# Optimization experiments

Measured on AMD Instinct MI355X. Metric: run time of the kernel, lower is better.

The kernel has to match this reference:

```python
import jax, jax.numpy as jnp
import numpy as np

B, T, N, D = 4, 12, 512, 128
L = 4            # max_lag + 1 lag encoders
H = D // 2       # lag-encoder hidden dim
THRESHOLD = 0.1


def setup_inputs() -> dict:
    key = jax.random.key(0)
    ks = jax.random.split(key, 10)
    s = 0.02
    return {
        "x":   jax.random.normal(ks[0], (B, T, N, D), dtype=jnp.float32),
        # lag encoders: Linear(D->H), ReLU, Linear(H->D), stacked over L lags
        "W1":  s * jax.random.normal(ks[1], (L, D, H), dtype=jnp.float32),
        "b1":  jnp.zeros((L, H), dtype=jnp.float32),
        "W2":  s * jax.random.normal(ks[2], (L, H, D), dtype=jnp.float32),
        "b2":  jnp.zeros((L, D), dtype=jnp.float32),
        # causal scorer: Linear(2D->D), ReLU, (Dropout=id in eval), Linear(D->1), Sigmoid
        "Ws1": s * jax.random.normal(ks[3], (2 * D, D), dtype=jnp.float32),
        "bs1": jnp.zeros((D,), dtype=jnp.float32),
        "Ws2": s * jax.random.normal(ks[4], (D, 1), dtype=jnp.float32),
        "bs2": jnp.zeros((1,), dtype=jnp.float32),
    }


def reference(x, W1, b1, W2, b2, Ws1, bs1, Ws2, bs2):
    Tdim = x.shape[1]
    # lagged slices x[:, T-1-lag] for lag in 0..L-1 (all lags active since T > max_lag)
    lags = jnp.stack([x[:, max(0, Tdim - 1 - l)] for l in range(L)], axis=1)  # (B,L,N,D)
    h = jax.nn.relu(jnp.einsum('blnd,ldh->blnh', lags, W1) + b1[None, :, None, :])
    enc = jnp.einsum('blnh,lhd->blnd', h, W2) + b2[None, :, None, :]          # (B,L,N,D)
    agg = enc.mean(axis=1)                                                    # (B,N,D)

    # pairwise causal scorer. cat([src, tgt]) @ Ws1 == src @ Ws1[:D] + tgt @ Ws1[D:],
    # avoiding the explicit (B,N,N,2D) concat.
    src_proj = jnp.einsum('bnd,dk->bnk', agg, Ws1[:D])   # (B,N,D)
    tgt_proj = jnp.einsum('bnd,dk->bnk', agg, Ws1[D:])   # (B,N,D)
    pre = src_proj[:, :, None, :] + tgt_proj[:, None, :, :] + bs1  # (B,N,N,D)
    score = jax.nn.sigmoid(jnp.einsum('bijd,d->bij', jax.nn.relu(pre), Ws2[:, 0]) + bs2[0])

    # threshold sparsification + remove self loops
    adj = jnp.where(score > THRESHOLD, score, 0.0)
    adj = adj * (1.0 - jnp.eye(N, dtype=adj.dtype))

    # multi-hop propagation and global max normalization per batch element
    a2 = jnp.matmul(adj, adj)
    a3 = jnp.matmul(a2, adj)
    enhanced = adj + 0.5 * a2 + 0.25 * a3
    mx = jnp.max(enhanced, axis=(-1, -2), keepdims=True)
    return enhanced / (mx + 1e-8)
```

## Files before the change

### kernel.cpp

```cpp
#include <hip/hip_runtime.h>
#include <math.h>

#define Bn 4
#define Tn 12
#define Nn 512
#define Dn 128
#define Ln 4
#define Hn 64
#define NNe (Nn*Nn)

typedef __attribute__((ext_vector_type(8))) short short8;
typedef __attribute__((ext_vector_type(4))) float f32x4;

__device__ __forceinline__ unsigned short f2bf(float f) {
    unsigned int u = __float_as_uint(f);
    unsigned int r = (u + 0x7FFF + ((u >> 16) & 1)) >> 16;
    return (unsigned short)r;
}
__device__ __forceinline__ float bf2f(unsigned short s) {
    return __uint_as_float(((unsigned int)s) << 16);
}

__global__ __launch_bounds__(256) void k_enc_a(
    const float* __restrict__ x, const float* __restrict__ W1, const float* __restrict__ b1,
    unsigned short* __restrict__ hb, unsigned int* __restrict__ maxslot)
{
    __shared__ __align__(16) unsigned short xA[32*136];
    __shared__ __align__(16) unsigned short w1T[64*136];
    int tid = threadIdx.x;
    int rg = blockIdx.x, lag = blockIdx.y;
    if (rg == 0 && lag == 0 && tid < Bn) maxslot[tid] = 0u;
    int r0 = rg * 32;
    int bb = r0 >> 9, n0 = r0 & 511;

    {
        const float4* xs = (const float4*)(x + ((size_t)(bb*Tn + (Tn-1-lag))*Nn + n0)*Dn);
        for (int v = tid; v < 1024; v += 256) {
            float4 f = xs[v];
            int row = v >> 5, c4 = v & 31;
            ushort4 o = { f2bf(f.x), f2bf(f.y), f2bf(f.z), f2bf(f.w) };
            *(ushort4*)&xA[row*136 + c4*4] = o;
        }
    }
    {
        int n = tid & 63, kq = tid >> 6;
        const float* Wp = W1 + (size_t)lag*Dn*Hn;
        #pragma unroll
        for (int r = 0; r < 4; ++r) {
            int k0 = (r*4 + kq)*8;
            unsigned short tmp[8];
            #pragma unroll
            for (int j = 0; j < 8; ++j) tmp[j] = f2bf(Wp[(size_t)(k0+j)*Hn + n]);
            *(short8*)&w1T[n*136 + k0] = *(const short8*)tmp;
        }
    }
    __syncthreads();

    int wv = __builtin_amdgcn_readfirstlane(tid >> 6);
    int lane = tid & 63;
    int wm = wv >> 1, wn = wv & 1;
    int m = lane & 15, q = lane >> 4;
    f32x4 acc[2] = {{0.f,0.f,0.f,0.f},{0.f,0.f,0.f,0.f}};
    #pragma unroll
    for (int ks = 0; ks < 4; ++ks) {
        short8 af = *(const short8*)&xA[(wm*16 + m)*136 + ks*32 + q*8];
        #pragma unroll
        for (int nt = 0; nt < 2; ++nt) {
            short8 bg = *(const short8*)&w1T[(wn*32 + nt*16 + m)*136 + ks*32 + q*8];
            acc[nt] = __builtin_amdgcn_mfma_f32_16x16x32_bf16(af, bg, acc[nt], 0, 0, 0);
        }
    }
    int colL = lane & 15, rq = lane >> 4;
    #pragma unroll
    for (int nt = 0; nt < 2; ++nt) {
        int ncol = wn*32 + nt*16 + colL;
        float bv = b1[lag*Hn + ncol];
        #pragma unroll
        for (int reg = 0; reg < 4; ++reg) {
            int rowL = wm*16 + rq*4 + reg;
            hb[(size_t)(r0+rowL)*256 + lag*64 + ncol] = f2bf(fmaxf(acc[nt][reg] + bv, 0.f));
        }
    }
}

__global__ __launch_bounds__(256) void k_enc_bc(
    const unsigned short* __restrict__ hb, const float* __restrict__ W2,
    const float* __restrict__ b2, const float* __restrict__ Ws1,
    const float* __restrict__ bs1,
    unsigned short* __restrict__ spb, unsigned short* __restrict__ tpb)
{
    __shared__ __align__(16) unsigned short hA[16*264];
    __shared__ __align__(16) unsigned short wT[64*264];
    __shared__ __align__(16) unsigned short aggA[16*136];
    int tid = threadIdx.x;
    int wv = __builtin_amdgcn_readfirstlane(tid >> 6);
    int lane = tid & 63;
    int r0 = blockIdx.x * 16;

    for (int v = tid; v < 512; v += 256) {
        int row = v >> 5, c = v & 31;
        *(short8*)&hA[row*264 + c*8] = *(const short8*)(hb + (size_t)(r0+row)*256 + c*8);
    }

    int m = lane & 15, q = lane >> 4;
    int colL = lane & 15, rq = lane >> 4;

    for (int ch = 0; ch < 2; ++ch) {
        __syncthreads();
        {
            int n = tid & 63, kq = tid >> 6;
            #pragma unroll
            for (int r = 0; r < 8; ++r) {
                int k0 = (r*4 + kq)*8;
                unsigned short tmp[8];
                #pragma unroll
                for (int j = 0; j < 8; ++j) tmp[j] = f2bf(W2[(size_t)(k0+j)*Dn + ch*64 + n]);
                *(short8*)&wT[n*264 + k0] = *(const short8*)tmp;
            }
        }
        __syncthreads();
        f32x4 acc = {0.f,0.f,0.f,0.f};
        #pragma unroll
        for (int ks = 0; ks < 8; ++ks) {
            short8 af = *(const short8*)&hA[m*264 + ks*32 + q*8];
            short8 bg = *(const short8*)&wT[(wv*16 + m)*264 + ks*32 + q*8];
            acc = __builtin_amdgcn_mfma_f32_16x16x32_bf16(af, bg, acc, 0, 0, 0);
        }
        int col = ch*64 + wv*16 + colL;
        float b2s = b2[col] + b2[Dn+col] + b2[2*Dn+col] + b2[3*Dn+col];
        #pragma unroll
        for (int reg = 0; reg < 4; ++reg)
            aggA[(rq*4+reg)*136 + col] = f2bf(0.25f*(acc[reg] + b2s));
    }

    for (int tgt = 0; tgt < 2; ++tgt) {
        __syncthreads();
        {
            int n = tid & 127, kq = tid >> 7;
            #pragma unroll
            for (int r = 0; r < 8; ++r) {
                int k0 = (r*2 + kq)*8;
                unsigned short tmp[8];
                #pragma unroll
                for (int j = 0; j < 8; ++j)
                    tmp[j] = f2bf(Ws1[(size_t)(tgt*Dn + k0 + j)*Dn + n]);
                *(short8*)&wT[n*136 + k0] = *(const short8*)tmp;
            }
        }
        __syncthreads();
        f32x4 acc[2] = {{0.f,0.f,0.f,0.f},{0.f,0.f,0.f,0.f}};
        #pragma unroll
        for (int ks = 0; ks < 4; ++ks) {
            short8 af = *(const short8*)&aggA[m*136 + ks*32 + q*8];
            #pragma unroll
            for (int nt = 0; nt < 2; ++nt) {
                short8 bg = *(const short8*)&wT[(wv*32 + nt*16 + m)*136 + ks*32 + q*8];
                acc[nt] = __builtin_amdgcn_mfma_f32_16x16x32_bf16(af, bg, acc[nt], 0, 0, 0);
            }
        }
        unsigned short* dst = tgt ? tpb : spb;
        #pragma unroll
        for (int nt = 0; nt < 2; ++nt) {
            int n = wv*32 + nt*16 + colL;
            float bv = tgt ? 0.f : bs1[n];
            #pragma unroll
            for (int reg = 0; reg < 4; ++reg)
                dst[(size_t)(r0 + rq*4 + reg)*Dn + n] = f2bf(acc[nt][reg] + bv);
        }
    }
}

__global__ __launch_bounds__(256) void k_score(
    const unsigned short* __restrict__ spb, const unsigned short* __restrict__ tpb,
    const float* __restrict__ Ws2, const float* __restrict__ bs2,
    unsigned short* __restrict__ adj_b, unsigned short* __restrict__ adj_bt)
{
    __shared__ float spl[64*132];
    __shared__ unsigned short tplT[Dn*72];
    int tid = threadIdx.x;
    int wv = __builtin_amdgcn_readfirstlane(tid >> 6);
    int lane = tid & 63;
    int bz = blockIdx.z;
    int i0b = blockIdx.y * 64, j0b = blockIdx.x * 64;
    const unsigned short* spr = spb + (size_t)bz*Nn*Dn;
    const unsigned short* tpr = tpb + (size_t)bz*Nn*Dn;

    for (int v = tid; v < 1024; v += 256) {
        int row = v >> 4, c = v & 15;
        const unsigned short* src = spr + (size_t)(i0b+row)*Dn + c*8;
        ushort4 u0 = *(const ushort4*)src;
        ushort4 u1 = *(const ushort4*)(src + 4);
        float4 f0 = { bf2f(u0.x), bf2f(u0.y), bf2f(u0.z), bf2f(u0.w) };
        float4 f1 = { bf2f(u1.x), bf2f(u1.y), bf2f(u1.z), bf2f(u1.w) };
        *(float4*)&spl[row*132 + c*8]     = f0;
        *(float4*)&spl[row*132 + c*8 + 4] = f1;
    }
    {
        int j = tid & 63, kq = tid >> 6;
        for (int p = 0; p < 4; ++p) {
            int k8 = p*4 + kq;
            short8 tv = *(const short8*)(tpr + (size_t)(j0b+j)*Dn + k8*8);
            #pragma unroll
            for (int t = 0; t < 8; ++t) tplT[(k8*8+t)*72 + j] = (unsigned short)tv[t];
        }
    }
    __syncthreads();

    int iq = lane >> 4, jq = lane & 15;
    int iw = wv*16 + iq*4;
    float acc[4][4] = {};
    for (int k8 = 0; k8 < 16; ++k8) {
        float4 wa = *(const float4*)(Ws2 + k8*8);
        float4 wb = *(const float4*)(Ws2 + k8*8 + 4);
        float4 sA[4], sB[4];
        #pragma unroll
        for (int ii = 0; ii < 4; ++ii) {
            sA[ii] = *(const float4*)&spl[(iw+ii)*132 + k8*8];
            sB[ii] = *(const float4*)&spl[(iw+ii)*132 + k8*8 + 4];
        }
        ushort4 t4[8];
        #pragma unroll
        for (int kk = 0; kk < 8; ++kk) t4[kk] = *(const ushort4*)&tplT[(k8*8+kk)*72 + jq*4];
        #pragma unroll
        for (int kk = 0; kk < 8; ++kk) {
            float w = (kk < 4) ? ((const float*)&wa)[kk] : ((const float*)&wb)[kk-4];
            float tv0 = bf2f(t4[kk].x), tv1 = bf2f(t4[kk].y);
            float tv2 = bf2f(t4[kk].z), tv3 = bf2f(t4[kk].w);
            #pragma unroll
            for (int ii = 0; ii < 4; ++ii) {
                float s = (kk < 4) ? ((const float*)&sA[ii])[kk] : ((const float*)&sB[ii])[kk-4];
                acc[ii][0] += fmaxf(s + tv0, 0.f)*w;
                acc[ii][1] += fmaxf(s + tv1, 0.f)*w;
                acc[ii][2] += fmaxf(s + tv2, 0.f)*w;
                acc[ii][3] += fmaxf(s + tv3, 0.f)*w;
            }
        }
    }
    float bsv = bs2[0];
    int i0 = i0b + iw;
    int j0 = j0b + jq*4;
    float vals[4][4];
    #pragma unroll
    for (int ii = 0; ii < 4; ++ii) {
        int i = i0 + ii;
        #pragma unroll
        for (int jj = 0; jj < 4; ++jj) {
            float z = acc[ii][jj] + bsv;
            float sc = 1.f/(1.f + __expf(-z));
            int j = j0 + jj;
            vals[ii][jj] = (sc > 0.1f && i != j) ? sc : 0.f;
        }
    }
    size_t base = (size_t)bz << 18;
    #pragma unroll
    for (int ii = 0; ii < 4; ++ii) {
        ushort4 rv = make_ushort4(f2bf(vals[ii][0]), f2bf(vals[ii][1]),
                                  f2bf(vals[ii][2]), f2bf(vals[ii][3]));
        *(ushort4*)(adj_b + base + (size_t)(i0+ii)*Nn + j0) = rv;
    }
    #pragma unroll
    for (int jj = 0; jj < 4; ++jj) {
        ushort4 cv = make_ushort4(f2bf(vals[0][jj]), f2bf(vals[1][jj]),
                                  f2bf(vals[2][jj]), f2bf(vals[3][jj]));
        *(ushort4*)(adj_bt + base + (size_t)(j0+jj)*Nn + i0) = cv;
    }
}

__global__ __launch_bounds__(256) void k_mm1(
    const unsigned short* __restrict__ adj_b, const unsigned short* __restrict__ adj_bt,
    unsigned short* __restrict__ a2b)
{
    __shared__ unsigned short Als[64*72];
    __shared__ unsigned short Bls[64*72];
    int tid = threadIdx.x;
    int wv = __builtin_amdgcn_readfirstlane(tid >> 6);
    int lane = tid & 63;
    int b = blockIdx.z, i0 = blockIdx.y*64, j0 = blockIdx.x*64;
    size_t base = (size_t)b << 18;
    const unsigned short* Ab = adj_b + base;
    const unsigned short* Bb = adj_bt + base;
    int wm = wv >> 1, wn = wv & 1;
    int m = lane & 15, q = lane >> 4;
    int sr = tid >> 2, sc = (tid & 3)*16;
    f32x4 acc[2][2];
    #pragma unroll
    for (int mt = 0; mt < 2; ++mt)
        #pragma unroll
        for (int nt = 0; nt < 2; ++nt) acc[mt][nt] = (f32x4){0.f,0.f,0.f,0.f};
    short8 pa0, pa1, pb0, pb1;
    pa0 = *(const short8*)(Ab + (size_t)(i0+sr)*Nn + sc);
    pa1 = *(const short8*)(Ab + (size_t)(i0+sr)*Nn + sc + 8);
    pb0 = *(const short8*)(Bb + (size_t)(j0+sr)*Nn + sc);
    pb1 = *(const short8*)(Bb + (size_t)(j0+sr)*Nn + sc + 8);
    for (int kt = 0; kt < 8; ++kt) {
        *(short8*)&Als[sr*72 + sc]     = pa0;
        *(short8*)&Als[sr*72 + sc + 8] = pa1;
        *(short8*)&Bls[sr*72 + sc]     = pb0;
        *(short8*)&Bls[sr*72 + sc + 8] = pb1;
        __syncthreads();
        if (kt < 7) {
            int k0 = (kt+1)*64;
            pa0 = *(const short8*)(Ab + (size_t)(i0+sr)*Nn + k0 + sc);
            pa1 = *(const short8*)(Ab + (size_t)(i0+sr)*Nn + k0 + sc + 8);
            pb0 = *(const short8*)(Bb + (size_t)(j0+sr)*Nn + k0 + sc);
            pb1 = *(const short8*)(Bb + (size_t)(j0+sr)*Nn + k0 + sc + 8);
        }
        #pragma unroll
        for (int ks = 0; ks < 2; ++ks) {
            short8 af[2], bg[2];
            #pragma unroll
            for (int mt = 0; mt < 2; ++mt) af[mt] = *(const short8*)&Als[(wm*32+mt*16+m)*72 + ks*32 + q*8];
            #pragma unroll
            for (int nt = 0; nt < 2; ++nt) bg[nt] = *(const short8*)&Bls[(wn*32+nt*16+m)*72 + ks*32 + q*8];
            #pragma unroll
            for (int mt = 0; mt < 2; ++mt)
                #pragma unroll
                for (int nt = 0; nt < 2; ++nt)
                    acc[mt][nt] = __builtin_amdgcn_mfma_f32_16x16x32_bf16(af[mt], bg[nt], acc[mt][nt], 0, 0, 0);
        }
        __syncthreads();
    }
    int col = lane & 15, rq = lane >> 4;
    #pragma unroll
    for (int mt = 0; mt < 2; ++mt)
        #pragma unroll
        for (int nt = 0; nt < 2; ++nt)
            #pragma unroll
            for (int reg = 0; reg < 4; ++reg) {
                int i = i0 + wm*32 + mt*16 + rq*4 + reg;
                int j = j0 + wn*32 + nt*16 + col;
                a2b[base + (size_t)i*Nn + j] = f2bf(acc[mt][nt][reg]);
            }
}

__global__ __launch_bounds__(256) void k_mm2(
    const unsigned short* __restrict__ adj_b, const unsigned short* __restrict__ adj_bt,
    const unsigned short* __restrict__ a2b,
    float* __restrict__ out, unsigned int* __restrict__ maxslot)
{
    __shared__ unsigned short Als[64*72];
    __shared__ unsigned short Bls[64*72];
    __shared__ float red[4];
    int tid = threadIdx.x;
    int wv = __builtin_amdgcn_readfirstlane(tid >> 6);
    int lane = tid & 63;
    int b = blockIdx.z, i0 = blockIdx.y*64, j0 = blockIdx.x*64;
    size_t base = (size_t)b << 18;
    const unsigned short* Ab = a2b + base;
    const unsigned short* Bb = adj_bt + base;
    int wm = wv >> 1, wn = wv & 1;
    int m = lane & 15, q = lane >> 4;
    int sr = tid >> 2, sc = (tid & 3)*16;
    f32x4 acc[2][2];
    #pragma unroll
    for (int mt = 0; mt < 2; ++mt)
        #pragma unroll
        for (int nt = 0; nt < 2; ++nt) acc[mt][nt] = (f32x4){0.f,0.f,0.f,0.f};
    short8 pa0, pa1, pb0, pb1;
    pa0 = *(const short8*)(Ab + (size_t)(i0+sr)*Nn + sc);
    pa1 = *(const short8*)(Ab + (size_t)(i0+sr)*Nn + sc + 8);
    pb0 = *(const short8*)(Bb + (size_t)(j0+sr)*Nn + sc);
    pb1 = *(const short8*)(Bb + (size_t)(j0+sr)*Nn + sc + 8);
    for (int kt = 0; kt < 8; ++kt) {
        *(short8*)&Als[sr*72 + sc]     = pa0;
        *(short8*)&Als[sr*72 + sc + 8] = pa1;
        *(short8*)&Bls[sr*72 + sc]     = pb0;
        *(short8*)&Bls[sr*72 + sc + 8] = pb1;
        __syncthreads();
        if (kt < 7) {
            int k0 = (kt+1)*64;
            pa0 = *(const short8*)(Ab + (size_t)(i0+sr)*Nn + k0 + sc);
            pa1 = *(const short8*)(Ab + (size_t)(i0+sr)*Nn + k0 + sc + 8);
            pb0 = *(const short8*)(Bb + (size_t)(j0+sr)*Nn + k0 + sc);
            pb1 = *(const short8*)(Bb + (size_t)(j0+sr)*Nn + k0 + sc + 8);
        }
        #pragma unroll
        for (int ks = 0; ks < 2; ++ks) {
            short8 af[2], bg[2];
            #pragma unroll
            for (int mt = 0; mt < 2; ++mt) af[mt] = *(const short8*)&Als[(wm*32+mt*16+m)*72 + ks*32 + q*8];
            #pragma unroll
            for (int nt = 0; nt < 2; ++nt) bg[nt] = *(const short8*)&Bls[(wn*32+nt*16+m)*72 + ks*32 + q*8];
            #pragma unroll
            for (int mt = 0; mt < 2; ++mt)
                #pragma unroll
                for (int nt = 0; nt < 2; ++nt)
                    acc[mt][nt] = __builtin_amdgcn_mfma_f32_16x16x32_bf16(af[mt], bg[nt], acc[mt][nt], 0, 0, 0);
        }
        __syncthreads();
    }
    int col = lane & 15, rq = lane >> 4;
    float lmax = 0.f;
    const unsigned short* adjp = adj_b + base;
    #pragma unroll
    for (int mt = 0; mt < 2; ++mt)
        #pragma unroll
        for (int nt = 0; nt < 2; ++nt)
            #pragma unroll
            for (int reg = 0; reg < 4; ++reg) {
                int i = i0 + wm*32 + mt*16 + rq*4 + reg;
                int j = j0 + wn*32 + nt*16 + col;
                size_t off = (size_t)i*Nn + j;
                float e = bf2f(adjp[off]) + 0.5f*bf2f(Ab[off]) + 0.25f*acc[mt][nt][reg];
                out[base + off] = e;
                lmax = fmaxf(lmax, e);
            }
    #pragma unroll
    for (int s = 1; s < 64; s <<= 1) lmax = fmaxf(lmax, __shfl_xor(lmax, s, 64));
    if (lane == 0) red[wv] = lmax;
    __syncthreads();
    if (tid == 0) {
        float mx = fmaxf(fmaxf(red[0], red[1]), fmaxf(red[2], red[3]));
        atomicMax(maxslot + b, __float_as_uint(mx));
    }
}

__global__ __launch_bounds__(256) void k_norm(float* __restrict__ out,
                                              const unsigned int* __restrict__ maxslot)
{
    int idx = blockIdx.x*256 + threadIdx.x;
    int b = idx >> 16;
    float m = __uint_as_float(maxslot[b]);
    float inv = 1.f/(m + 1e-8f);
    float4* p = (float4*)out + idx;
    float4 v = *p;
    v.x *= inv; v.y *= inv; v.z *= inv; v.w *= inv;
    *p = v;
}

extern "C" void kernel_launch(void* const* d_in, const int* in_sizes, int n_in,
                              void* d_out, int out_size, void* d_ws, size_t ws_size,
                              hipStream_t stream) {
    const float* x   = (const float*)d_in[0];
    const float* W1  = (const float*)d_in[1];
    const float* b1  = (const float*)d_in[2];
    const float* W2  = (const float*)d_in[3];
    const float* b2  = (const float*)d_in[4];
    const float* Ws1 = (const float*)d_in[5];
    const float* bs1 = (const float*)d_in[6];
    const float* Ws2 = (const float*)d_in[7];
    const float* bs2 = (const float*)d_in[8];
    float* out = (float*)d_out;

    unsigned char* wsb = (unsigned char*)d_ws;
    unsigned short* spb    = (unsigned short*)(wsb);
    unsigned short* tpb    = (unsigned short*)(wsb + (512u<<10));
    unsigned short* adj_b  = (unsigned short*)(wsb + (1024u<<10));
    unsigned short* adj_bt = (unsigned short*)(wsb + (3072u<<10));
    unsigned short* a2b    = (unsigned short*)(wsb + (5120u<<10));
    unsigned int*   maxslot= (unsigned int*)(wsb + (7168u<<10));
    unsigned short* hb     = (unsigned short*)(wsb + (7172u<<10));

    k_enc_a <<<dim3(64, 4),   256, 0, stream>>>(x, W1, b1, hb, maxslot);
    k_enc_bc<<<dim3(128),     256, 0, stream>>>(hb, W2, b2, Ws1, bs1, spb, tpb);
    k_score <<<dim3(8, 8, Bn),256, 0, stream>>>(spb, tpb, Ws2, bs2, adj_b, adj_bt);
    k_mm1   <<<dim3(8, 8, Bn),256, 0, stream>>>(adj_b, adj_bt, a2b);
    k_mm2   <<<dim3(8, 8, Bn),256, 0, stream>>>(adj_b, adj_bt, a2b, out, maxslot);
    k_norm  <<<dim3(1024),    256, 0, stream>>>(out, maxslot);
}
```

Baseline: 124.4 us.

## Fuse all stages into one cooperative persistent kernel with grid syncs

Replaces six separate kernel launches with a single cooperative kernel of 256 blocks that runs the encoder, scorer, two adjacency matmuls and normalization as phases separated by grid-wide syncs. The encoder's first layer is also fused with the second, so the hidden activations stay in LDS instead of making a round trip through global memory. The aim is to remove launch gaps and inter-kernel tail effects. In exchange, only 128 blocks do work in the encoder phase, and each grid sync adds barrier cost.

```diff
diff --git a/kernel.cpp b/kernel.cpp
--- a/kernel.cpp
+++ b/kernel.cpp
@@ -1,5 +1,8 @@
 #include <hip/hip_runtime.h>
+#include <hip/hip_cooperative_groups.h>
 #include <math.h>
+
+namespace cg = cooperative_groups;
 
 #define Bn 4
 #define Tn 12
@@ -7,7 +10,6 @@
 #define Dn 128
 #define Ln 4
 #define Hn 64
-#define NNe (Nn*Nn)
 
 typedef __attribute__((ext_vector_type(8))) short short8;
 typedef __attribute__((ext_vector_type(4))) float f32x4;
@@ -21,411 +23,380 @@
     return __uint_as_float(((unsigned int)s) << 16);
 }
 
-__global__ __launch_bounds__(256) void k_enc_a(
-    const float* __restrict__ x, const float* __restrict__ W1, const float* __restrict__ b1,
-    unsigned short* __restrict__ hb, unsigned int* __restrict__ maxslot)
+__global__ __launch_bounds__(256) void k_all(
+    const float* __restrict__ x,  const float* __restrict__ W1, const float* __restrict__ b1,
+    const float* __restrict__ W2, const float* __restrict__ b2,
+    const float* __restrict__ Ws1, const float* __restrict__ bs1,
+    const float* __restrict__ Ws2, const float* __restrict__ bs2,
+    unsigned short* __restrict__ spb, unsigned short* __restrict__ tpb,
+    unsigned short* __restrict__ adj_b, unsigned short* __restrict__ adj_bt,
+    unsigned short* __restrict__ a2b,
+    unsigned int* __restrict__ maxslot, float* __restrict__ out)
 {
-    __shared__ __align__(16) unsigned short xA[32*136];
-    __shared__ __align__(16) unsigned short w1T[64*136];
-    int tid = threadIdx.x;
-    int rg = blockIdx.x, lag = blockIdx.y;
-    if (rg == 0 && lag == 0 && tid < Bn) maxslot[tid] = 0u;
-    int r0 = rg * 32;
-    int bb = r0 >> 9, n0 = r0 & 511;
+    __shared__ __align__(16) unsigned char ldsraw[52224];
+    cg::grid_group gg = cg::this_grid();
+    int tid  = threadIdx.x;
+    int bid  = blockIdx.x;
+    int wv   = __builtin_amdgcn_readfirstlane(tid >> 6);
+    int lane = tid & 63;
+
+    if (bid == 0 && tid < Bn)
+        __hip_atomic_store(maxslot + tid, 0u, __ATOMIC_RELAXED, __HIP_MEMORY_SCOPE_AGENT);
+
+    if (bid < 128) {
+        unsigned short* hA   = (unsigned short*)ldsraw;
+        unsigned short* wT   = (unsigned short*)(ldsraw + 8448);
+        unsigned short* aggA = (unsigned short*)(ldsraw + 43264);
+        unsigned short* xA   = aggA;
+        int r0 = bid * 16;
+        int bb = r0 >> 9, n0 = r0 & 511;
+        int m = lane & 15, q = lane >> 4;
+        int colL = lane & 15, rq = lane >> 4;
+
+        for (int lag = 0; lag < Ln; ++lag) {
+            __syncthreads();
+            {
+                const float4* xs = (const float4*)(x + ((size_t)(bb*Tn + (Tn-1-lag))*Nn + n0)*Dn);
+                for (int v = tid; v < 512; v += 256) {
+                    float4 f = xs[v];
+                    int row = v >> 5, c4 = v & 31;
+                    ushort4 o = { f2bf(f.x), f2bf(f.y), f2bf(f.z), f2bf(f.w) };
+                    *(ushort4*)&xA[row*136 + c4*4] = o;
+                }
+            }
+            {
+                int n = tid & 63, kq = tid >> 6;
+                const float* Wp = W1 + (size_t)lag*Dn*Hn;
+                #pragma unroll
+                for (int r = 0; r < 4; ++r) {
+                    int k0 = (r*4 + kq)*8;
+                    unsigned short tmp[8];
+                    #pragma unroll
+                    for (int j = 0; j < 8; ++j) tmp[j] = f2bf(Wp[(size_t)(k0+j)*Hn + n]);
+                    *(short8*)&wT[n*136 + k0] = *(const short8*)tmp;
+                }
+            }
+            __syncthreads();
+            f32x4 acc = {0.f,0.f,0.f,0.f};
+            #pragma unroll
+            for (int ks = 0; ks < 4; ++ks) {
+                short8 af = *(const short8*)&xA[m*136 + ks*32 + q*8];
+                short8 bg = *(const short8*)&wT[(wv*16 + m)*136 + ks*32 + q*8];
+                acc = __builtin_amdgcn_mfma_f32_16x16x32_bf16(af, bg, acc, 0, 0, 0);
+            }
+            int ncol = wv*16 + colL;
+            float bv = b1[lag*Hn + ncol];
+            #pragma unroll
+            for (int reg = 0; reg < 4; ++reg)
+                hA[(rq*4+reg)*264 + lag*64 + ncol] = f2bf(fmaxf(acc[reg] + bv, 0.f));
+        }
+
+        for (int ch = 0; ch < 2; ++ch) {
+            __syncthreads();
+            {
+                int n = tid & 63, kq = tid >> 6;
+                #pragma unroll
+                for (int r = 0; r < 8; ++r) {
+                    int k0 = (r*4 + kq)*8;
+                    unsigned short tmp[8];
+                    #pragma unroll
+                    for (int j = 0; j < 8; ++j) tmp[j] = f2bf(W2[(size_t)(k0+j)*Dn + ch*64 + n]);
+                    *(short8*)&wT[n*264 + k0] = *(const short8*)tmp;
+                }
+            }
+            __syncthreads();
+            f32x4 acc = {0.f,0.f,0.f,0.f};
+            #pragma unroll
+            for (int ks = 0; ks < 8; ++ks) {
+                short8 af = *(const short8*)&hA[m*264 + ks*32 + q*8];
+                short8 bg = *(const short8*)&wT[(wv*16 + m)*264 + ks*32 + q*8];
+                acc = __builtin_amdgcn_mfma_f32_16x16x32_bf16(af, bg, acc, 0, 0, 0);
+            }
+            int col = ch*64 + wv*16 + colL;
+            float b2s = b2[col] + b2[Dn+col] + b2[2*Dn+col] + b2[3*Dn+col];
+            #pragma unroll
+            for (int reg = 0; reg < 4; ++reg)
+                aggA[(rq*4+reg)*136 + col] = f2bf(0.25f*(acc[reg] + b2s));
+        }
+
+        for (int tgt = 0; tgt < 2; ++tgt) {
+            __syncthreads();
+            {
+                int n = tid & 127, kq = tid >> 7;
+                #pragma unroll
+                for (int r = 0; r < 8; ++r) {
+                    int k0 = (r*2 + kq)*8;
+                    unsigned short tmp[8];
+                    #pragma unroll
+                    for (int j = 0; j < 8; ++j)
+                        tmp[j] = f2bf(Ws1[(size_t)(tgt*Dn + k0 + j)*Dn + n]);
+                    *(short8*)&wT[n*136 + k0] = *(const short8*)tmp;
+                }
+            }
+            __syncthreads();
+            f32x4 acc[2] = {{0.f,0.f,0.f,0.f},{0.f,0.f,0.f,0.f}};
+            #pragma unroll
+            for (int ks = 0; ks < 4; ++ks) {
+                short8 af = *(const short8*)&aggA[m*136 + ks*32 + q*8];
+                #pragma unroll
+                for (int nt = 0; nt < 2; ++nt) {
+                    short8 bg = *(const short8*)&wT[(wv*32 + nt*16 + m)*136 + ks*32 + q*8];
+                    acc[nt] = __builtin_amdgcn_mfma_f32_16x16x32_bf16(af, bg, acc[nt], 0, 0, 0);
+                }
+            }
+            unsigned short* dst = tgt ? tpb : spb;
+            #pragma unroll
+            for (int nt = 0; nt < 2; ++nt) {
+                int n = wv*32 + nt*16 + colL;
+                float bv = tgt ? 0.f : bs1[n];
+                #pragma unroll
+                for (int reg = 0; reg < 4; ++reg)
+                    dst[(size_t)(r0 + rq*4 + reg)*Dn + n] = f2bf(acc[nt][reg] + bv);
+            }
+        }
+    }
+    gg.sync();
 
     {
-        const float4* xs = (const float4*)(x + ((size_t)(bb*Tn + (Tn-1-lag))*Nn + n0)*Dn);
+        float* spl = (float*)ldsraw;
+        unsigned short* tplT = (unsigned short*)(ldsraw + 33792);
+        int bz = bid >> 6, i0b = ((bid >> 3) & 7) * 64, j0b = (bid & 7) * 64;
+        const unsigned short* spr = spb + (size_t)bz*Nn*Dn;
+        const unsigned short* tpr = tpb + (size_t)bz*Nn*Dn;
+
         for (int v = tid; v < 1024; v += 256) {
-            float4 f = xs[v];
-            int row = v >> 5, c4 = v & 31;
-            ushort4 o = { f2bf(f.x), f2bf(f.y), f2bf(f.z), f2bf(f.w) };
-            *(ushort4*)&xA[row*136 + c4*4] = o;
+            int row = v >> 4, c = v & 15;
+            const unsigned short* src = spr + (size_t)(i0b+row)*Dn + c*8;
+            ushort4 u0 = *(const ushort4*)src;
+            ushort4 u1 = *(const ushort4*)(src + 4);
+            float4 f0 = { bf2f(u0.x), bf2f(u0.y), bf2f(u0.z), bf2f(u0.w) };
+            float4 f1 = { bf2f(u1.x), bf2f(u1.y), bf2f(u1.z), bf2f(u1.w) };
+            *(float4*)&spl[row*132 + c*8]     = f0;
+            *(float4*)&spl[row*132 + c*8 + 4] = f1;
+        }
+        {
+            int j = tid & 63, kq = tid >> 6;
+            for (int p = 0; p < 4; ++p) {
+                int k8 = p*4 + kq;
+                short8 tv = *(const short8*)(tpr + (size_t)(j0b+j)*Dn + k8*8);
+                #pragma unroll
+                for (int t = 0; t < 8; ++t) tplT[(k8*8+t)*72 + j] = (unsigned short)tv[t];
+            }
+        }
+        __syncthreads();
+
+        int iq = lane >> 4, jq = lane & 15;
+        int iw = wv*16 + iq*4;
+        float acc[4][4] = {};
+        for (int k8 = 0; k8 < 16; ++k8) {
+            float4 wa = *(const float4*)(Ws2 + k8*8);
+            float4 wb = *(const float4*)(Ws2 + k8*8 + 4);
+            float4 sA[4], sB[4];
+            #pragma unroll
+            for (int ii = 0; ii < 4; ++ii) {
+                sA[ii] = *(const float4*)&spl[(iw+ii)*132 + k8*8];
+                sB[ii] = *(const float4*)&spl[(iw+ii)*132 + k8*8 + 4];
+            }
+            ushort4 t4[8];
+            #pragma unroll
+            for (int kk = 0; kk < 8; ++kk) t4[kk] = *(const ushort4*)&tplT[(k8*8+kk)*72 + jq*4];
+            #pragma unroll
+            for (int kk = 0; kk < 8; ++kk) {
+                float w = (kk < 4) ? ((const float*)&wa)[kk] : ((const float*)&wb)[kk-4];
+                float tv0 = bf2f(t4[kk].x), tv1 = bf2f(t4[kk].y);
+                float tv2 = bf2f(t4[kk].z), tv3 = bf2f(t4[kk].w);
+                #pragma unroll
+                for (int ii = 0; ii < 4; ++ii) {
+                    float s = (kk < 4) ? ((const float*)&sA[ii])[kk] : ((const float*)&sB[ii])[kk-4];
+                    acc[ii][0] += fmaxf(s + tv0, 0.f)*w;
+                    acc[ii][1] += fmaxf(s + tv1, 0.f)*w;
+                    acc[ii][2] += fmaxf(s + tv2, 0.f)*w;
+                    acc[ii][3] += fmaxf(s + tv3, 0.f)*w;
+                }
+            }
+        }
+        float bsv = bs2[0];
+        int i0 = i0b + iw;
+        int j0 = j0b + jq*4;
+        float vals[4][4];
+        #pragma unroll
+        for (int ii = 0; ii < 4; ++ii) {
+            int i = i0 + ii;
+            #pragma unroll
+            for (int jj = 0; jj < 4; ++jj) {
+                float z = acc[ii][jj] + bsv;
+                float sc = 1.f/(1.f + __expf(-z));
+                int j = j0 + jj;
+                vals[ii][jj] = (sc > 0.1f && i != j) ? sc : 0.f;
+            }
+        }
+        size_t base = (size_t)bz << 18;
+        #pragma unroll
+        for (int ii = 0; ii < 4; ++ii) {
+            ushort4 rv = make_ushort4(f2bf(vals[ii][0]), f2bf(vals[ii][1]),
+                                      f2bf(vals[ii][2]), f2bf(vals[ii][3]));
+            *(ushort4*)(adj_b + base + (size_t)(i0+ii)*Nn + j0) = rv;
+        }
+        #pragma unroll
+        for (int jj = 0; jj < 4; ++jj) {
+            ushort4 cv = make_ushort4(f2bf(vals[0][jj]), f2bf(vals[1][jj]),
+                                      f2bf(vals[2][jj]), f2bf(vals[3][jj]));
+            *(ushort4*)(adj_bt + base + (size_t)(j0+jj)*Nn + i0) = cv;
         }
     }
+    gg.sync();
+
     {
-        int n = tid & 63, kq = tid >> 6;
-        const float* Wp = W1 + (size_t)lag*Dn*Hn;
-        #pragma unroll
-        for (int r = 0; r < 4; ++r) {
-            int k0 = (r*4 + kq)*8;
-            unsigned short tmp[8];
-            #pragma unroll
-            for (int j = 0; j < 8; ++j) tmp[j] = f2bf(Wp[(size_t)(k0+j)*Hn + n]);
-            *(short8*)&w1T[n*136 + k0] = *(const short8*)tmp;
-        }
+        unsigned short* Als = (unsigned short*)ldsraw;
+        unsigned short* Bls = (unsigned short*)(ldsraw + 9216);
+        int bz = bid >> 6, i0 = ((bid >> 3) & 7)*64, j0 = (bid & 7)*64;
+        size_t base = (size_t)bz << 18;
+        const unsigned short* Ab = adj_b + base;
+        const unsigned short* Bb = adj_bt + base;
+        int wm = wv >> 1, wn = wv & 1;
+        int m = lane & 15, q = lane >> 4;
+        int sr = tid >> 2, sc = (tid & 3)*16;
+        f32x4 acc[2][2];
+        #pragma unroll
+        for (int mt = 0; mt < 2; ++mt)
+            #pragma unroll
+            for (int nt = 0; nt < 2; ++nt) acc[mt][nt] = (f32x4){0.f,0.f,0.f,0.f};
+        short8 pa0 = *(const short8*)(Ab + (size_t)(i0+sr)*Nn + sc);
+        short8 pa1 = *(const short8*)(Ab + (size_t)(i0+sr)*Nn + sc + 8);
+        short8 pb0 = *(const short8*)(Bb + (size_t)(j0+sr)*Nn + sc);
+        short8 pb1 = *(const short8*)(Bb + (size_t)(j0+sr)*Nn + sc + 8);
+        for (int kt = 0; kt < 8; ++kt) {
+            *(short8*)&Als[sr*72 + sc]     = pa0;
+            *(short8*)&Als[sr*72 + sc + 8] = pa1;
+            *(short8*)&Bls[sr*72 + sc]     = pb0;
+            *(short8*)&Bls[sr*72 + sc + 8] = pb1;
+            __syncthreads();
+            if (kt < 7) {
+                int k0 = (kt+1)*64;
+                pa0 = *(const short8*)(Ab + (size_t)(i0+sr)*Nn + k0 + sc);
+                pa1 = *(const short8*)(Ab + (size_t)(i0+sr)*Nn + k0 + sc + 8);
+                pb0 = *(const short8*)(Bb + (size_t)(j0+sr)*Nn + k0 + sc);
+                pb1 = *(const short8*)(Bb + (size_t)(j0+sr)*Nn + k0 + sc + 8);
+            }
+            #pragma unroll
+            for (int ks = 0; ks < 2; ++ks) {
+                short8 af[2], bg[2];
+                #pragma unroll
+                for (int mt = 0; mt < 2; ++mt) af[mt] = *(const short8*)&Als[(wm*32+mt*16+m)*72 + ks*32 + q*8];
+                #pragma unroll
+                for (int nt = 0; nt < 2; ++nt) bg[nt] = *(const short8*)&Bls[(wn*32+nt*16+m)*72 + ks*32 + q*8];
+                #pragma unroll
+                for (int mt = 0; mt < 2; ++mt)
+                    #pragma unroll
+                    for (int nt = 0; nt < 2; ++nt)
+                        acc[mt][nt] = __builtin_amdgcn_mfma_f32_16x16x32_bf16(af[mt], bg[nt], acc[mt][nt], 0, 0, 0);
+            }
+            __syncthreads();
+        }
+        int col = lane & 15, rq = lane >> 4;
+        #pragma unroll
+        for (int mt = 0; mt < 2; ++mt)
+            #pragma unroll
+            for (int nt = 0; nt < 2; ++nt)
+                #pragma unroll
+                for (int reg = 0; reg < 4; ++reg) {
+                    int i = i0 + wm*32 + mt*16 + rq*4 + reg;
+                    int j = j0 + wn*32 + nt*16 + col;
+                    a2b[base + (size_t)i*Nn + j] = f2bf(acc[mt][nt][reg]);
+                }
     }
-    __syncthreads();
-
-    int wv = __builtin_amdgcn_readfirstlane(tid >> 6);
-    int lane = tid & 63;
-    int wm = wv >> 1, wn = wv & 1;
-    int m = lane & 15, q = lane >> 4;
-    f32x4 acc[2] = {{0.f,0.f,0.f,0.f},{0.f,0.f,0.f,0.f}};
-    #pragma unroll
-    for (int ks = 0; ks < 4; ++ks) {
-        short8 af = *(const short8*)&xA[(wm*16 + m)*136 + ks*32 + q*8];
-        #pragma unroll
-        for (int nt = 0; nt < 2; ++nt) {
-            short8 bg = *(const short8*)&w1T[(wn*32 + nt*16 + m)*136 + ks*32 + q*8];
-            acc[nt] = __builtin_amdgcn_mfma_f32_16x16x32_bf16(af, bg, acc[nt], 0, 0, 0);
-        }
+    gg.sync();
+
+    {
+        unsigned short* Als = (unsigned short*)ldsraw;
+        unsigned short* Bls = (unsigned short*)(ldsraw + 9216);
+        float* red = (float*)(ldsraw + 18432);
+        int bz = bid >> 6, i0 = ((bid >> 3) & 7)*64, j0 = (bid & 7)*64;
+        size_t base = (size_t)bz << 18;
+        const unsigned short* Ab = a2b + base;
+        const unsigned short* Bb = adj_bt + base;
+        int wm = wv >> 1, wn = wv & 1;
+        int m = lane & 15, q = lane >> 4;
+        int sr = tid >> 2, sc = (tid & 3)*16;
+        f32x4 acc[2][2];
+        #pragma unroll
+        for (int mt = 0; mt < 2; ++mt)
+            #pragma unroll
+            for (int nt = 0; nt < 2; ++nt) acc[mt][nt] = (f32x4){0.f,0.f,0.f,0.f};
+        short8 pa0 = *(const short8*)(Ab + (size_t)(i0+sr)*Nn + sc);
+        short8 pa1 = *(const short8*)(Ab + (size_t)(i0+sr)*Nn + sc + 8);
+        short8 pb0 = *(const short8*)(Bb + (size_t)(j0+sr)*Nn + sc);
+        short8 pb1 = *(const short8*)(Bb + (size_t)(j0+sr)*Nn + sc + 8);
+        for (int kt = 0; kt < 8; ++kt) {
+            *(short8*)&Als[sr*72 + sc]     = pa0;
+            *(short8*)&Als[sr*72 + sc + 8] = pa1;
+            *(short8*)&Bls[sr*72 + sc]     = pb0;
+            *(short8*)&Bls[sr*72 + sc + 8] = pb1;
+            __syncthreads();
+            if (kt < 7) {
+                int k0 = (kt+1)*64;
+                pa0 = *(const short8*)(Ab + (size_t)(i0+sr)*Nn + k0 + sc);
+                pa1 = *(const short8*)(Ab + (size_t)(i0+sr)*Nn + k0 + sc + 8);
+                pb0 = *(const short8*)(Bb + (size_t)(j0+sr)*Nn + k0 + sc);
+                pb1 = *(const short8*)(Bb + (size_t)(j0+sr)*Nn + k0 + sc + 8);
+            }
+            #pragma unroll
+            for (int ks = 0; ks < 2; ++ks) {
+                short8 af[2], bg[2];
+                #pragma unroll
+                for (int mt = 0; mt < 2; ++mt) af[mt] = *(const short8*)&Als[(wm*32+mt*16+m)*72 + ks*32 + q*8];
+                #pragma unroll
+                for (int nt = 0; nt < 2; ++nt) bg[nt] = *(const short8*)&Bls[(wn*32+nt*16+m)*72 + ks*32 + q*8];
+                #pragma unroll
+                for (int mt = 0; mt < 2; ++mt)
+                    #pragma unroll
+                    for (int nt = 0; nt < 2; ++nt)
+                        acc[mt][nt] = __builtin_amdgcn_mfma_f32_16x16x32_bf16(af[mt], bg[nt], acc[mt][nt], 0, 0, 0);
+            }
+            __syncthreads();
+        }
+        int col = lane & 15, rq = lane >> 4;
+        float lmax = 0.f;
+        const unsigned short* adjp = adj_b + base;
+        #pragma unroll
+        for (int mt = 0; mt < 2; ++mt)
+            #pragma unroll
+            for (int nt = 0; nt < 2; ++nt)
+                #pragma unroll
+                for (int reg = 0; reg < 4; ++reg) {
+                    int i = i0 + wm*32 + mt*16 + rq*4 + reg;
+                    int j = j0 + wn*32 + nt*16 + col;
+                    size_t off = (size_t)i*Nn + j;
+                    float e = bf2f(adjp[off]) + 0.5f*bf2f(Ab[off]) + 0.25f*acc[mt][nt][reg];
+                    acc[mt][nt][reg] = e;
+                    lmax = fmaxf(lmax, e);
+                }
+        #pragma unroll
+        for (int s = 1; s < 64; s <<= 1) lmax = fmaxf(lmax, __shfl_xor(lmax, s, 64));
+        if (lane == 0) red[wv] = lmax;
+        __syncthreads();
+        if (tid == 0) {
+            float mx = fmaxf(fmaxf(red[0], red[1]), fmaxf(red[2], red[3]));
+            atomicMax(maxslot + bz, __float_as_uint(mx));
+        }
+        gg.sync();
+        if (tid == 0) {
+            unsigned int mu = __hip_atomic_load(maxslot + bz, __ATOMIC_RELAXED, __HIP_MEMORY_SCOPE_AGENT);
+            red[0] = 1.f / (__uint_as_float(mu) + 1e-8f);
+        }
+        __syncthreads();
+        float inv = red[0];
+        #pragma unroll
+        for (int mt = 0; mt < 2; ++mt)
+            #pragma unroll
+            for (int nt = 0; nt < 2; ++nt)
+                #pragma unroll
+                for (int reg = 0; reg < 4; ++reg) {
+                    int i = i0 + wm*32 + mt*16 + rq*4 + reg;
+                    int j = j0 + wn*32 + nt*16 + col;
+                    out[base + (size_t)i*Nn + j] = acc[mt][nt][reg] * inv;
+                }
     }
-    int colL = lane & 15, rq = lane >> 4;
-    #pragma unroll
-    for (int nt = 0; nt < 2; ++nt) {
-        int ncol = wn*32 + nt*16 + colL;
-        float bv = b1[lag*Hn + ncol];
-        #pragma unroll
-        for (int reg = 0; reg < 4; ++reg) {
-            int rowL = wm*16 + rq*4 + reg;
-            hb[(size_t)(r0+rowL)*256 + lag*64 + ncol] = f2bf(fmaxf(acc[nt][reg] + bv, 0.f));
-        }
-    }
-}
-
-__global__ __launch_bounds__(256) void k_enc_bc(
-    const unsigned short* __restrict__ hb, const float* __restrict__ W2,
-    const float* __restrict__ b2, const float* __restrict__ Ws1,
-    const float* __restrict__ bs1,
-    unsigned short* __restrict__ spb, unsigned short* __restrict__ tpb)
-{
-    __shared__ __align__(16) unsigned short hA[16*264];
-    __shared__ __align__(16) unsigned short wT[64*264];
-    __shared__ __align__(16) unsigned short aggA[16*136];
-    int tid = threadIdx.x;
-    int wv = __builtin_amdgcn_readfirstlane(tid >> 6);
-    int lane = tid & 63;
-    int r0 = blockIdx.x * 16;
-
-    for (int v = tid; v < 512; v += 256) {
-        int row = v >> 5, c = v & 31;
-        *(short8*)&hA[row*264 + c*8] = *(const short8*)(hb + (size_t)(r0+row)*256 + c*8);
-    }
-
-    int m = lane & 15, q = lane >> 4;
-    int colL = lane & 15, rq = lane >> 4;
-
-    for (int ch = 0; ch < 2; ++ch) {
-        __syncthreads();
-        {
-            int n = tid & 63, kq = tid >> 6;
-            #pragma unroll
-            for (int r = 0; r < 8; ++r) {
-                int k0 = (r*4 + kq)*8;
-                unsigned short tmp[8];
-                #pragma unroll
-                for (int j = 0; j < 8; ++j) tmp[j] = f2bf(W2[(size_t)(k0+j)*Dn + ch*64 + n]);
-                *(short8*)&wT[n*264 + k0] = *(const short8*)tmp;
-            }
-        }
-        __syncthreads();
-        f32x4 acc = {0.f,0.f,0.f,0.f};
-        #pragma unroll
-        for (int ks = 0; ks < 8; ++ks) {
-            short8 af = *(const short8*)&hA[m*264 + ks*32 + q*8];
-            short8 bg = *(const short8*)&wT[(wv*16 + m)*264 + ks*32 + q*8];
-            acc = __builtin_amdgcn_mfma_f32_16x16x32_bf16(af, bg, acc, 0, 0, 0);
-        }
-        int col = ch*64 + wv*16 + colL;
-        float b2s = b2[col] + b2[Dn+col] + b2[2*Dn+col] + b2[3*Dn+col];
-        #pragma unroll
-        for (int reg = 0; reg < 4; ++reg)
-            aggA[(rq*4+reg)*136 + col] = f2bf(0.25f*(acc[reg] + b2s));
-    }
-
-    for (int tgt = 0; tgt < 2; ++tgt) {
-        __syncthreads();
-        {
-            int n = tid & 127, kq = tid >> 7;
-            #pragma unroll
-            for (int r = 0; r < 8; ++r) {
-                int k0 = (r*2 + kq)*8;
-                unsigned short tmp[8];
-                #pragma unroll
-                for (int j = 0; j < 8; ++j)
-                    tmp[j] = f2bf(Ws1[(size_t)(tgt*Dn + k0 + j)*Dn + n]);
-                *(short8*)&wT[n*136 + k0] = *(const short8*)tmp;
-            }
-        }
-        __syncthreads();
-        f32x4 acc[2] = {{0.f,0.f,0.f,0.f},{0.f,0.f,0.f,0.f}};
-        #pragma unroll
-        for (int ks = 0; ks < 4; ++ks) {
-            short8 af = *(const short8*)&aggA[m*136 + ks*32 + q*8];
-            #pragma unroll
-            for (int nt = 0; nt < 2; ++nt) {
-                short8 bg = *(const short8*)&wT[(wv*32 + nt*16 + m)*136 + ks*32 + q*8];
-                acc[nt] = __builtin_amdgcn_mfma_f32_16x16x32_bf16(af, bg, acc[nt], 0, 0, 0);
-            }
-        }
-        unsigned short* dst = tgt ? tpb : spb;
-        #pragma unroll
-        for (int nt = 0; nt < 2; ++nt) {
-            int n = wv*32 + nt*16 + colL;
-            float bv = tgt ? 0.f : bs1[n];
-            #pragma unroll
-            for (int reg = 0; reg < 4; ++reg)
-                dst[(size_t)(r0 + rq*4 + reg)*Dn + n] = f2bf(acc[nt][reg] + bv);
-        }
-    }
-}
-
-__global__ __launch_bounds__(256) void k_score(
-    const unsigned short* __restrict__ spb, const unsigned short* __restrict__ tpb,
-    const float* __restrict__ Ws2, const float* __restrict__ bs2,
-    unsigned short* __restrict__ adj_b, unsigned short* __restrict__ adj_bt)
-{
-    __shared__ float spl[64*132];
-    __shared__ unsigned short tplT[Dn*72];
-    int tid = threadIdx.x;
-    int wv = __builtin_amdgcn_readfirstlane(tid >> 6);
-    int lane = tid & 63;
-    int bz = blockIdx.z;
-    int i0b = blockIdx.y * 64, j0b = blockIdx.x * 64;
-    const unsigned short* spr = spb + (size_t)bz*Nn*Dn;
-    const unsigned short* tpr = tpb + (size_t)bz*Nn*Dn;
-
-    for (int v = tid; v < 1024; v += 256) {
-        int row = v >> 4, c = v & 15;
-        const unsigned short* src = spr + (size_t)(i0b+row)*Dn + c*8;
-        ushort4 u0 = *(const ushort4*)src;
-        ushort4 u1 = *(const ushort4*)(src + 4);
-        float4 f0 = { bf2f(u0.x), bf2f(u0.y), bf2f(u0.z), bf2f(u0.w) };
-        float4 f1 = { bf2f(u1.x), bf2f(u1.y), bf2f(u1.z), bf2f(u1.w) };
-        *(float4*)&spl[row*132 + c*8]     = f0;
-        *(float4*)&spl[row*132 + c*8 + 4] = f1;
-    }
-    {
-        int j = tid & 63, kq = tid >> 6;
-        for (int p = 0; p < 4; ++p) {
-            int k8 = p*4 + kq;
-            short8 tv = *(const short8*)(tpr + (size_t)(j0b+j)*Dn + k8*8);
-            #pragma unroll
-            for (int t = 0; t < 8; ++t) tplT[(k8*8+t)*72 + j] = (unsigned short)tv[t];
-        }
-    }
-    __syncthreads();
-
-    int iq = lane >> 4, jq = lane & 15;
-    int iw = wv*16 + iq*4;
-    float acc[4][4] = {};
-    for (int k8 = 0; k8 < 16; ++k8) {
-        float4 wa = *(const float4*)(Ws2 + k8*8);
-        float4 wb = *(const float4*)(Ws2 + k8*8 + 4);
-        float4 sA[4], sB[4];
-        #pragma unroll
-        for (int ii = 0; ii < 4; ++ii) {
-            sA[ii] = *(const float4*)&spl[(iw+ii)*132 + k8*8];
-            sB[ii] = *(const float4*)&spl[(iw+ii)*132 + k8*8 + 4];
-        }
-        ushort4 t4[8];
-        #pragma unroll
-        for (int kk = 0; kk < 8; ++kk) t4[kk] = *(const ushort4*)&tplT[(k8*8+kk)*72 + jq*4];
-        #pragma unroll
-        for (int kk = 0; kk < 8; ++kk) {
-            float w = (kk < 4) ? ((const float*)&wa)[kk] : ((const float*)&wb)[kk-4];
-            float tv0 = bf2f(t4[kk].x), tv1 = bf2f(t4[kk].y);
-            float tv2 = bf2f(t4[kk].z), tv3 = bf2f(t4[kk].w);
-            #pragma unroll
-            for (int ii = 0; ii < 4; ++ii) {
-                float s = (kk < 4) ? ((const float*)&sA[ii])[kk] : ((const float*)&sB[ii])[kk-4];
-                acc[ii][0] += fmaxf(s + tv0, 0.f)*w;
-                acc[ii][1] += fmaxf(s + tv1, 0.f)*w;
-                acc[ii][2] += fmaxf(s + tv2, 0.f)*w;
-                acc[ii][3] += fmaxf(s + tv3, 0.f)*w;
-            }
-        }
-    }
-    float bsv = bs2[0];
-    int i0 = i0b + iw;
-    int j0 = j0b + jq*4;
-    float vals[4][4];
-    #pragma unroll
-    for (int ii = 0; ii < 4; ++ii) {
-        int i = i0 + ii;
-        #pragma unroll
-        for (int jj = 0; jj < 4; ++jj) {
-            float z = acc[ii][jj] + bsv;
-            float sc = 1.f/(1.f + __expf(-z));
-            int j = j0 + jj;
-            vals[ii][jj] = (sc > 0.1f && i != j) ? sc : 0.f;
-        }
-    }
-    size_t base = (size_t)bz << 18;
-    #pragma unroll
-    for (int ii = 0; ii < 4; ++ii) {
-        ushort4 rv = make_ushort4(f2bf(vals[ii][0]), f2bf(vals[ii][1]),
-                                  f2bf(vals[ii][2]), f2bf(vals[ii][3]));
-        *(ushort4*)(adj_b + base + (size_t)(i0+ii)*Nn + j0) = rv;
-    }
-    #pragma unroll
-    for (int jj = 0; jj < 4; ++jj) {
-        ushort4 cv = make_ushort4(f2bf(vals[0][jj]), f2bf(vals[1][jj]),
-                                  f2bf(vals[2][jj]), f2bf(vals[3][jj]));
-        *(ushort4*)(adj_bt + base + (size_t)(j0+jj)*Nn + i0) = cv;
-    }
-}
-
-__global__ __launch_bounds__(256) void k_mm1(
-    const unsigned short* __restrict__ adj_b, const unsigned short* __restrict__ adj_bt,
-    unsigned short* __restrict__ a2b)
-{
-    __shared__ unsigned short Als[64*72];
-    __shared__ unsigned short Bls[64*72];
-    int tid = threadIdx.x;
-    int wv = __builtin_amdgcn_readfirstlane(tid >> 6);
-    int lane = tid & 63;
-    int b = blockIdx.z, i0 = blockIdx.y*64, j0 = blockIdx.x*64;
-    size_t base = (size_t)b << 18;
-    const unsigned short* Ab = adj_b + base;
-    const unsigned short* Bb = adj_bt + base;
-    int wm = wv >> 1, wn = wv & 1;
-    int m = lane & 15, q = lane >> 4;
-    int sr = tid >> 2, sc = (tid & 3)*16;
-    f32x4 acc[2][2];
-    #pragma unroll
-    for (int mt = 0; mt < 2; ++mt)
-        #pragma unroll
-        for (int nt = 0; nt < 2; ++nt) acc[mt][nt] = (f32x4){0.f,0.f,0.f,0.f};
-    short8 pa0, pa1, pb0, pb1;
-    pa0 = *(const short8*)(Ab + (size_t)(i0+sr)*Nn + sc);
-    pa1 = *(const short8*)(Ab + (size_t)(i0+sr)*Nn + sc + 8);
-    pb0 = *(const short8*)(Bb + (size_t)(j0+sr)*Nn + sc);
-    pb1 = *(const short8*)(Bb + (size_t)(j0+sr)*Nn + sc + 8);
-    for (int kt = 0; kt < 8; ++kt) {
-        *(short8*)&Als[sr*72 + sc]     = pa0;
-        *(short8*)&Als[sr*72 + sc + 8] = pa1;
-        *(short8*)&Bls[sr*72 + sc]     = pb0;
-        *(short8*)&Bls[sr*72 + sc + 8] = pb1;
-        __syncthreads();
-        if (kt < 7) {
-            int k0 = (kt+1)*64;
-            pa0 = *(const short8*)(Ab + (size_t)(i0+sr)*Nn + k0 + sc);
-            pa1 = *(const short8*)(Ab + (size_t)(i0+sr)*Nn + k0 + sc + 8);
-            pb0 = *(const short8*)(Bb + (size_t)(j0+sr)*Nn + k0 + sc);
-            pb1 = *(const short8*)(Bb + (size_t)(j0+sr)*Nn + k0 + sc + 8);
-        }
-        #pragma unroll
-        for (int ks = 0; ks < 2; ++ks) {
-            short8 af[2], bg[2];
-            #pragma unroll
-            for (int mt = 0; mt < 2; ++mt) af[mt] = *(const short8*)&Als[(wm*32+mt*16+m)*72 + ks*32 + q*8];
-            #pragma unroll
-            for (int nt = 0; nt < 2; ++nt) bg[nt] = *(const short8*)&Bls[(wn*32+nt*16+m)*72 + ks*32 + q*8];
-            #pragma unroll
-            for (int mt = 0; mt < 2; ++mt)
-                #pragma unroll
-                for (int nt = 0; nt < 2; ++nt)
-                    acc[mt][nt] = __builtin_amdgcn_mfma_f32_16x16x32_bf16(af[mt], bg[nt], acc[mt][nt], 0, 0, 0);
-        }
-        __syncthreads();
-    }
-    int col = lane & 15, rq = lane >> 4;
-    #pragma unroll
-    for (int mt = 0; mt < 2; ++mt)
-        #pragma unroll
-        for (int nt = 0; nt < 2; ++nt)
-            #pragma unroll
-            for (int reg = 0; reg < 4; ++reg) {
-                int i = i0 + wm*32 + mt*16 + rq*4 + reg;
-                int j = j0 + wn*32 + nt*16 + col;
-                a2b[base + (size_t)i*Nn + j] = f2bf(acc[mt][nt][reg]);
-            }
-}
-
-__global__ __launch_bounds__(256) void k_mm2(
-    const unsigned short* __restrict__ adj_b, const unsigned short* __restrict__ adj_bt,
-    const unsigned short* __restrict__ a2b,
-    float* __restrict__ out, unsigned int* __restrict__ maxslot)
-{
-    __shared__ unsigned short Als[64*72];
-    __shared__ unsigned short Bls[64*72];
-    __shared__ float red[4];
-    int tid = threadIdx.x;
-    int wv = __builtin_amdgcn_readfirstlane(tid >> 6);
-    int lane = tid & 63;
-    int b = blockIdx.z, i0 = blockIdx.y*64, j0 = blockIdx.x*64;
-    size_t base = (size_t)b << 18;
-    const unsigned short* Ab = a2b + base;
-    const unsigned short* Bb = adj_bt + base;
-    int wm = wv >> 1, wn = wv & 1;
-    int m = lane & 15, q = lane >> 4;
-    int sr = tid >> 2, sc = (tid & 3)*16;
-    f32x4 acc[2][2];
-    #pragma unroll
-    for (int mt = 0; mt < 2; ++mt)
-        #pragma unroll
-        for (int nt = 0; nt < 2; ++nt) acc[mt][nt] = (f32x4){0.f,0.f,0.f,0.f};
-    short8 pa0, pa1, pb0, pb1;
-    pa0 = *(const short8*)(Ab + (size_t)(i0+sr)*Nn + sc);
-    pa1 = *(const short8*)(Ab + (size_t)(i0+sr)*Nn + sc + 8);
-    pb0 = *(const short8*)(Bb + (size_t)(j0+sr)*Nn + sc);
-    pb1 = *(const short8*)(Bb + (size_t)(j0+sr)*Nn + sc + 8);
-    for (int kt = 0; kt < 8; ++kt) {
-        *(short8*)&Als[sr*72 + sc]     = pa0;
-        *(short8*)&Als[sr*72 + sc + 8] = pa1;
-        *(short8*)&Bls[sr*72 + sc]     = pb0;
-        *(short8*)&Bls[sr*72 + sc + 8] = pb1;
-        __syncthreads();
-        if (kt < 7) {
-            int k0 = (kt+1)*64;
-            pa0 = *(const short8*)(Ab + (size_t)(i0+sr)*Nn + k0 + sc);
-            pa1 = *(const short8*)(Ab + (size_t)(i0+sr)*Nn + k0 + sc + 8);
-            pb0 = *(const short8*)(Bb + (size_t)(j0+sr)*Nn + k0 + sc);
-            pb1 = *(const short8*)(Bb + (size_t)(j0+sr)*Nn + k0 + sc + 8);
-        }
-        #pragma unroll
-        for (int ks = 0; ks < 2; ++ks) {
-            short8 af[2], bg[2];
-            #pragma unroll
-            for (int mt = 0; mt < 2; ++mt) af[mt] = *(const short8*)&Als[(wm*32+mt*16+m)*72 + ks*32 + q*8];
-            #pragma unroll
-            for (int nt = 0; nt < 2; ++nt) bg[nt] = *(const short8*)&Bls[(wn*32+nt*16+m)*72 + ks*32 + q*8];
-            #pragma unroll
-            for (int mt = 0; mt < 2; ++mt)
-                #pragma unroll
-                for (int nt = 0; nt < 2; ++nt)
-                    acc[mt][nt] = __builtin_amdgcn_mfma_f32_16x16x32_bf16(af[mt], bg[nt], acc[mt][nt], 0, 0, 0);
-        }
-        __syncthreads();
-    }
-    int col = lane & 15, rq = lane >> 4;
-    float lmax = 0.f;
-    const unsigned short* adjp = adj_b + base;
-    #pragma unroll
-    for (int mt = 0; mt < 2; ++mt)
-        #pragma unroll
-        for (int nt = 0; nt < 2; ++nt)
-            #pragma unroll
-            for (int reg = 0; reg < 4; ++reg) {
-                int i = i0 + wm*32 + mt*16 + rq*4 + reg;
-                int j = j0 + wn*32 + nt*16 + col;
-                size_t off = (size_t)i*Nn + j;
-                float e = bf2f(adjp[off]) + 0.5f*bf2f(Ab[off]) + 0.25f*acc[mt][nt][reg];
-                out[base + off] = e;
-                lmax = fmaxf(lmax, e);
-            }
-    #pragma unroll
-    for (int s = 1; s < 64; s <<= 1) lmax = fmaxf(lmax, __shfl_xor(lmax, s, 64));
-    if (lane == 0) red[wv] = lmax;
-    __syncthreads();
-    if (tid == 0) {
-        float mx = fmaxf(fmaxf(red[0], red[1]), fmaxf(red[2], red[3]));
-        atomicMax(maxslot + b, __float_as_uint(mx));
-    }
-}
-
-__global__ __launch_bounds__(256) void k_norm(float* __restrict__ out,
-                                              const unsigned int* __restrict__ maxslot)
-{
-    int idx = blockIdx.x*256 + threadIdx.x;
-    int b = idx >> 16;
-    float m = __uint_as_float(maxslot[b]);
-    float inv = 1.f/(m + 1e-8f);
-    float4* p = (float4*)out + idx;
-    float4 v = *p;
-    v.x *= inv; v.y *= inv; v.z *= inv; v.w *= inv;
-    *p = v;
 }
 
 extern "C" void kernel_launch(void* const* d_in, const int* in_sizes, int n_in,
@@ -449,12 +420,13 @@
     unsigned short* adj_bt = (unsigned short*)(wsb + (3072u<<10));
     unsigned short* a2b    = (unsigned short*)(wsb + (5120u<<10));
     unsigned int*   maxslot= (unsigned int*)(wsb + (7168u<<10));
-    unsigned short* hb     = (unsigned short*)(wsb + (7172u<<10));
-
-    k_enc_a <<<dim3(64, 4),   256, 0, stream>>>(x, W1, b1, hb, maxslot);
-    k_enc_bc<<<dim3(128),     256, 0, stream>>>(hb, W2, b2, Ws1, bs1, spb, tpb);
-    k_score <<<dim3(8, 8, Bn),256, 0, stream>>>(spb, tpb, Ws2, bs2, adj_b, adj_bt);
-    k_mm1   <<<dim3(8, 8, Bn),256, 0, stream>>>(adj_b, adj_bt, a2b);
-    k_mm2   <<<dim3(8, 8, Bn),256, 0, stream>>>(adj_b, adj_bt, a2b, out, maxslot);
-    k_norm  <<<dim3(1024),    256, 0, stream>>>(out, maxslot);
+
+    void* args[] = {
+        (void*)&x, (void*)&W1, (void*)&b1, (void*)&W2, (void*)&b2,
+        (void*)&Ws1, (void*)&bs1, (void*)&Ws2, (void*)&bs2,
+        (void*)&spb, (void*)&tpb, (void*)&adj_b, (void*)&adj_bt, (void*)&a2b,
+        (void*)&maxslot, (void*)&out
+    };
+    (void)hipLaunchCooperativeKernel((const void*)k_all, dim3(256), dim3(256),
+                                     args, 0, stream);
 }
```

Measured after the change: 239.4 us. 1.92x slower.
